# Optimization experiments

Measured on AMD Instinct MI355X. Metric: run time of the kernel, lower is better.

Reference implementation:

```python
import jax, jax.numpy as jnp
import numpy as np

GROUP = 64
DIM = 4096
N_HEADS = 32
N_KV = 8
HEAD_DIM = DIM // N_HEADS  # 128
N_REP = N_HEADS // N_KV    # 4
B = 1
S = 2048
THETA = 1e6


def _pack_q40(rng, out_f, in_f):
    """Random int4 weights packed Q4_0 style (two nibbles per int8) + per-group scales."""
    q = rng.integers(-7, 8, size=(out_f * in_f,)).reshape(-1, 2, GROUP)
    packed = ((q[:, 0] << 4) | (q[:, 1] & 15)).astype(np.int8)  # [out*in/group/2, group]
    scale = (np.abs(rng.standard_normal((out_f * in_f // GROUP, 1))) * 0.01 + 1e-3).astype(np.float32)
    return jnp.asarray(packed), jnp.asarray(scale)


def dequantize_q40(w, scale, shape):
    """Faithful port of torch dequantize_q40: arithmetic shifts sign-extend nibbles."""
    msb = jnp.right_shift(w, 4)                          # high nibble, sign-extended
    lsb = jnp.right_shift(jnp.left_shift(w, 4), 4)       # low nibble, sign-extended
    grp = jnp.concatenate([msb, lsb], axis=1).reshape(-1, GROUP)  # hstack then view(-1, group)
    return (grp.astype(scale.dtype) * scale).reshape(shape)


def setup_inputs() -> dict:
    rng = np.random.default_rng(0)
    wq, sq = _pack_q40(rng, N_HEADS * HEAD_DIM, DIM)
    wk, sk = _pack_q40(rng, N_KV * HEAD_DIM, DIM)
    wv, sv = _pack_q40(rng, N_KV * HEAD_DIM, DIM)
    wo, so = _pack_q40(rng, DIM, N_HEADS * HEAD_DIM)
    x = jnp.asarray(rng.standard_normal((B, S, DIM)), jnp.float32)
    inv_freq = 1.0 / (THETA ** (np.arange(0, HEAD_DIM, 2, dtype=np.float64) / HEAD_DIM))
    ang = np.outer(np.arange(S, dtype=np.float64), inv_freq)  # [S, HEAD_DIM/2]
    cos = jnp.asarray(np.cos(ang), jnp.float32)
    sin = jnp.asarray(np.sin(ang), jnp.float32)
    causal = np.triu(np.ones((S, S), dtype=bool), k=1)
    mask = jnp.asarray(np.where(causal, -1e9, 0.0), jnp.float32)
    return dict(x=x, wq=wq, sq=sq, wk=wk, sk=sk, wv=wv, sv=sv, wo=wo, so=so,
                cos=cos, sin=sin, mask=mask)


def _rotate_half(t):
    h = t.shape[-1] // 2
    return jnp.concatenate([-t[..., h:], t[..., :h]], axis=-1)


def reference(x, wq, sq, wk, sk, wv, sv, wo, so, cos, sin, mask):
    # Dequant-then-matmul QKV projections (weights stored as [out, in])
    Wq = dequantize_q40(wq, sq, (N_HEADS * HEAD_DIM, DIM))
    Wk = dequantize_q40(wk, sk, (N_KV * HEAD_DIM, DIM))
    Wv = dequantize_q40(wv, sv, (N_KV * HEAD_DIM, DIM))
    Wo = dequantize_q40(wo, so, (DIM, N_HEADS * HEAD_DIM))

    xq = (x @ Wq.T).reshape(B, S, N_HEADS, HEAD_DIM)
    xk = (x @ Wk.T).reshape(B, S, N_KV, HEAD_DIM)
    xv = (x @ Wv.T).reshape(B, S, N_KV, HEAD_DIM)

    # RoPE (rotate-half convention): cos/sin are [S, HEAD_DIM/2] -> cat to [S, HEAD_DIM]
    cosf = jnp.concatenate([cos, cos], axis=-1)[:, None, :]  # [S, 1, HEAD_DIM]
    sinf = jnp.concatenate([sin, sin], axis=-1)[:, None, :]
    xq = xq * cosf + _rotate_half(xq) * sinf
    xk = xk * cosf + _rotate_half(xk) * sinf

    # start_pos == 0 prefill: keys/values are the freshly projected xk/xv
    # GQA: repeat_interleave over the kv-head dim
    keys = jnp.repeat(xk, N_REP, axis=2)    # [B, S, N_HEADS, HEAD_DIM]
    values = jnp.repeat(xv, N_REP, axis=2)

    scores = jnp.einsum('bqhd,bkhd->bhqk', xq, keys) / np.float32(np.sqrt(HEAD_DIM))
    scores = scores + mask  # additive causal mask broadcast over [B, H]
    attn = jax.nn.softmax(scores, axis=-1)
    out = jnp.einsum('bhqk,bkhd->bqhd', attn, values).reshape(B, S, N_HEADS * HEAD_DIM)
    return out @ Wo.T
```

## Files before the change

### kernel.cpp

```cpp
#include <hip/hip_runtime.h>
#include <stdint.h>

#define DIMX 4096
#define NH   32
#define NKV  8
#define HD   128
#define SEQ  2048
#define QKVD 6144

typedef _Float16 h16;
typedef __attribute__((ext_vector_type(8))) _Float16 h16x8;
typedef __attribute__((ext_vector_type(4))) _Float16 h16x4;
typedef __attribute__((ext_vector_type(4))) float   f32x4;

__device__ __forceinline__ void gload_lds16(const void* g, void* l) {
  __builtin_amdgcn_global_load_lds(
      (const __attribute__((address_space(1))) void*)g,
      (__attribute__((address_space(3))) void*)l, 16, 0, 0);
}

template <int CTRL>
__device__ __forceinline__ float dpp_mv(float x) {
  int y = __builtin_amdgcn_mov_dpp(__builtin_bit_cast(int, x), CTRL, 0xF, 0xF, true);
  return __builtin_bit_cast(float, y);
}
__device__ __forceinline__ float red16_max(float x) {
  x = fmaxf(x, dpp_mv<0xB1>(x));
  x = fmaxf(x, dpp_mv<0x1B>(x));
  x = fmaxf(x, dpp_mv<0x141>(x));
  x = fmaxf(x, dpp_mv<0x140>(x));
  return x;
}
__device__ __forceinline__ float red16_sum(float x) {
  x += dpp_mv<0xB1>(x);
  x += dpp_mv<0x1B>(x);
  x += dpp_mv<0x141>(x);
  x += dpp_mv<0x140>(x);
  return x;
}

template <int PERM>
__device__ __forceinline__ void dq_unit(const void* __restrict__ w, const float* __restrict__ sc,
                                        h16* __restrict__ out, int u, int flag) {
  uint32_t b4;
  if (flag) {
    const int4 t = *(const int4*)((const int*)w + 4 * u);
    b4 = (uint32_t)(t.x & 0xFF) | ((uint32_t)(t.y & 0xFF) << 8) |
         ((uint32_t)(t.z & 0xFF) << 16) | ((uint32_t)(t.w & 0xFF) << 24);
  } else {
    b4 = ((const uint32_t*)w)[u];
  }
  int r = u >> 4;
  int p = (u & 15) * 4;
  float shi = sc[2 * r], slo = sc[2 * r + 1];
  h16x4 hi, lo;
#pragma unroll
  for (int j = 0; j < 4; ++j) {
    int by = (int)((b4 >> (8 * j)) & 0xFF);
    int hn = (by << 24) >> 28;
    int ln = (by << 28) >> 28;
    hi[j] = (h16)((float)hn * shi);
    lo[j] = (h16)((float)ln * slo);
  }
  size_t base;
  if (PERM) {
    int row  = r >> 5;
    int rowp = (row & ~127) | (((row & 63) << 1) | ((row >> 6) & 1));
    base = ((size_t)rowp << 12) + (size_t)((r & 31) << 7);
  } else {
    base = (size_t)r << 7;
  }
  *(h16x4*)(out + base + p)      = hi;
  *(h16x4*)(out + base + 64 + p) = lo;
}

#define U_WQ 2097152
#define U_WK 524288
#define U_WV 524288
#define U_WO 2097152

__global__ __launch_bounds__(256) void prep_all(
    const void* __restrict__ wq, const float* __restrict__ sq,
    const void* __restrict__ wk, const float* __restrict__ sk,
    const void* __restrict__ wv, const float* __restrict__ sv,
    const void* __restrict__ wo, const float* __restrict__ so,
    const float4* __restrict__ x,
    h16* __restrict__ Wqkv, h16* __restrict__ Wo, h16x4* __restrict__ xb) {
  __shared__ int sfl;
  if (threadIdx.x == 0) {
    int ok = 1;
    const int* wi = (const int*)wq;
    for (int i = 0; i < 64; ++i) {
      int v = wi[i];
      if (v < -128 || v > 127) ok = 0;
    }
    sfl = ok;
  }
  __syncthreads();
  const int fl = sfl;
  int u = blockIdx.x * 256 + threadIdx.x;
  if (u < U_WQ) { dq_unit<1>(wq, sq, Wqkv, u, fl); return; }
  u -= U_WQ;
  if (u < U_WK) { dq_unit<1>(wk, sk, Wqkv + 16777216, u, fl); return; }
  u -= U_WK;
  if (u < U_WV) { dq_unit<0>(wv, sv, Wqkv + 20971520, u, fl); return; }
  u -= U_WV;
  if (u < U_WO) { dq_unit<0>(wo, so, Wo, u, fl); return; }
  u -= U_WO;
  {
    float4 v = x[u];
    h16x4 o;
    o.x = (h16)v.x; o.y = (h16)v.y; o.z = (h16)v.z; o.w = (h16)v.w;
    xb[u] = o;
  }
}

template <typename OutT, int NT, int MODE>
__global__ __launch_bounds__(256) void gemm_bt(
    const h16* __restrict__ A, const h16* __restrict__ B,
    OutT* __restrict__ C, int M, int N, int K,
    const float* __restrict__ cosb, const float* __restrict__ sinb,
    h16* __restrict__ vt) {
  constexpr int BN = NT * 32;
  constexpr int SSZ = 128 * 64 + BN * 64;
  __shared__ __attribute__((aligned(16))) h16 SMEM[SSZ];
  h16* As = SMEM;
  h16* Bs = SMEM + 128 * 64;

  const int tid  = threadIdx.x;
  const int wv   = tid >> 6, lane = tid & 63;
  const int wr   = wv >> 1,  wc   = wv & 1;
  const int quad = lane >> 4, l15 = lane & 15;
  const int m0 = blockIdx.y * 128, n0 = blockIdx.x * BN;

  f32x4 acc[4][NT];
#pragma unroll
  for (int i = 0; i < 4; ++i)
#pragma unroll
    for (int j = 0; j < NT; ++j) acc[i][j] = (f32x4){0.f, 0.f, 0.f, 0.f};

  const h16* Ab = A + (size_t)m0 * K;
  const h16* Bb = B + (size_t)n0 * K;

  for (int k0 = 0; k0 < K; k0 += 64) {
    __syncthreads();
#pragma unroll
    for (int i = 0; i < 4; ++i) {
      int c = i * 256 + tid;
      int row = c >> 3, cs = c & 7, g = cs ^ (row & 7);
      gload_lds16(Ab + (size_t)row * K + k0 + g * 8, (char*)As + c * 16);
    }
#pragma unroll
    for (int i = 0; i < NT; ++i) {
      int c = i * 256 + tid;
      int row = c >> 3, cs = c & 7, g = cs ^ (row & 7);
      gload_lds16(Bb + (size_t)row * K + k0 + g * 8, (char*)Bs + c * 16);
    }
    __syncthreads();

#pragma unroll
    for (int ks = 0; ks < 2; ++ks) {
      h16x8 af[4], bfr[NT];
#pragma unroll
      for (int mt = 0; mt < 4; ++mt) {
        int row = wr * 64 + mt * 16 + l15;
        af[mt] = *(const h16x8*)&As[row * 64 + (((ks * 4 + quad) ^ (row & 7)) * 8)];
      }
#pragma unroll
      for (int nt = 0; nt < NT; ++nt) {
        int row = wc * (NT * 16) + nt * 16 + l15;
        bfr[nt] = *(const h16x8*)&Bs[row * 64 + (((ks * 4 + quad) ^ (row & 7)) * 8)];
      }
#pragma unroll
      for (int mt = 0; mt < 4; ++mt)
#pragma unroll
        for (int nt = 0; nt < NT; ++nt)
          acc[mt][nt] = __builtin_amdgcn_mfma_f32_16x16x32_f16(af[mt], bfr[nt], acc[mt][nt], 0, 0, 0);
    }
  }

#pragma unroll
  for (int mt = 0; mt < 4; ++mt)
#pragma unroll
    for (int nt = 0; nt < NT; ++nt)
#pragma unroll
      for (int r = 0; r < 4; ++r) {
        int row = m0 + wr * 64 + mt * 16 + quad * 4 + r;
        int col = n0 + wc * (NT * 16) + nt * 16 + l15;
        C[(size_t)row * N + col] = (OutT)acc[mt][nt][r];
      }
}

__global__ __launch_bounds__(512, 2) void gemm192_qkv(
    const h16* __restrict__ A, const h16* __restrict__ B, h16* __restrict__ C,
    const float* __restrict__ cosb, const float* __restrict__ sinb,
    h16* __restrict__ vt) {
  constexpr int K = DIMX;
  __shared__ __attribute__((aligned(16))) h16 SM[57344];

  const int tid  = threadIdx.x;
  const int w    = tid >> 6, lane = tid & 63;
  const int wr   = w >> 1, wc = w & 1;
  const int quad = lane >> 4, l15 = lane & 15;
  const int m0 = blockIdx.y * 256, n0 = blockIdx.x * 192;

  const h16* Ab = A + (size_t)m0 * K;
  const h16* Bb = B + (size_t)n0 * K;
  const int srow = tid >> 3;
  const int sg8  = ((tid & 7) ^ (srow & 7)) * 8;

  f32x4 acc[2][2][2][3];
#pragma unroll
  for (int a = 0; a < 2; ++a)
#pragma unroll
    for (int b = 0; b < 2; ++b)
#pragma unroll
      for (int mt = 0; mt < 2; ++mt)
#pragma unroll
        for (int nt = 0; nt < 3; ++nt) acc[a][b][mt][nt] = (f32x4){0.f, 0.f, 0.f, 0.f};

  h16x8 af[2][2];
  h16x8 bf[2][3][2];

#define STG(sl_, tile_) do {                                                        \
    const h16* g_ = ((sl_) < 4) ? (Ab + (size_t)((sl_) * 64) * K)                   \
                                : (Bb + (size_t)(((sl_) - 4) * 64) * K);            \
    char* d_ = (char*)(SM + ((tile_) & 1) * 28672 + (sl_) * 4096);                  \
    gload_lds16(g_ + (size_t)srow * K + (tile_) * 64 + sg8, d_ + tid * 16);         \
  } while (0)

#define LDA_(tile_, a_) do {                                                        \
    const h16* s_ = SM + ((tile_) & 1) * 28672 + wr * 4096;                         \
    _Pragma("unroll") for (int mt = 0; mt < 2; ++mt)                                \
    _Pragma("unroll") for (int ks = 0; ks < 2; ++ks) {                              \
      int row_ = (a_) * 32 + mt * 16 + l15;                                         \
      af[mt][ks] = *(const h16x8*)&s_[row_ * 64 + (((ks * 4 + quad) ^ (row_ & 7)) * 8)]; \
    }                                                                               \
  } while (0)

#define LDB_(tile_, b_) do {                                                        \
    const h16* s_ = SM + ((tile_) & 1) * 28672 + 16384;                             \
    _Pragma("unroll") for (int nt = 0; nt < 3; ++nt)                                \
    _Pragma("unroll") for (int ks = 0; ks < 2; ++ks) {                              \
      int row_ = (b_) * 96 + wc * 48 + nt * 16 + l15;                               \
      bf[b_][nt][ks] = *(const h16x8*)&s_[row_ * 64 + (((ks * 4 + quad) ^ (row_ & 7)) * 8)]; \
    }                                                                               \
  } while (0)

#define MMA_(a_, b_) do {                                                           \
    __builtin_amdgcn_s_setprio(1);                                                  \
    _Pragma("unroll") for (int mt = 0; mt < 2; ++mt)                                \
    _Pragma("unroll") for (int nt = 0; nt < 3; ++nt)                                \
    _Pragma("unroll") for (int ks = 0; ks < 2; ++ks)                                \
      acc[a_][b_][mt][nt] = __builtin_amdgcn_mfma_f32_16x16x32_f16(                 \
          af[mt][ks], bf[b_][nt][ks], acc[a_][b_][mt][nt], 0, 0, 0);                \
    __builtin_amdgcn_s_setprio(0);                                                  \
  } while (0)

#define CFENCE asm volatile("" ::: "memory")
#define BARX do { CFENCE; __builtin_amdgcn_s_barrier(); CFENCE; } while (0)
#define LG0  asm volatile("s_waitcnt lgkmcnt(0)" ::: "memory")
#define LKH8 asm volatile("s_waitcnt lgkmcnt(8)" ::: "memory")
#define VM5  asm volatile("s_waitcnt vmcnt(5)" ::: "memory")
#define VM0  asm volatile("s_waitcnt vmcnt(0)" ::: "memory")

  const int NT2 = K >> 6;

  STG(4, 0); STG(5, 0); STG(6, 0); STG(0, 0); STG(1, 0);
  STG(2, 0); STG(3, 0);
  STG(4, 1); STG(5, 1); STG(6, 1); STG(0, 1); STG(1, 1);
  VM5;
  BARX;

  for (int t = 0; t < NT2; ++t) {
    const int tp1 = (t + 1 < NT2) ? t + 1 : NT2 - 1;
    const int tp2 = (t + 2 < NT2) ? t + 2 : NT2 - 1;
    LDA_(t, 0); LDB_(t, 0);
    STG(2, tp1); STG(3, tp1);
    LKH8;
    BARX; LG0; MMA_(0, 0); BARX;
    LDB_(t, 1);
    STG(4, tp2);
    BARX; LG0; MMA_(0, 1); BARX;
    LDA_(t, 1);
    STG(5, tp2);
    BARX; LG0; MMA_(1, 1); BARX;
    STG(6, tp2); STG(0, tp2); STG(1, tp2);
    BARX; MMA_(1, 0); VM5; BARX;
  }
  VM0;

#pragma unroll
  for (int a = 0; a < 2; ++a)
#pragma unroll
    for (int b = 0; b < 2; ++b)
#pragma unroll
      for (int mt = 0; mt < 2; ++mt)
#pragma unroll
        for (int nt = 0; nt < 3; ++nt) {
          const int cb   = n0 + b * 96 + wc * 48 + nt * 16;
          const int row0 = m0 + wr * 64 + a * 32 + mt * 16 + quad * 4;
          if (cb >= 5120) {
            const int dcol = cb + l15 - 5120;
            h16x4 vvv;
#pragma unroll
            for (int r = 0; r < 4; ++r) vvv[r] = (h16)acc[a][b][mt][nt][r];
            *(h16x4*)(vt + (size_t)dcol * SEQ + row0) = vvv;
          } else {
            const int col = cb + l15;
            const int j   = (col & 127) >> 1;
            const float sgn = (col & 1) ? 1.f : -1.f;
#pragma unroll
            for (int r = 0; r < 4; ++r) {
              float own = acc[a][b][mt][nt][r];
              float par = dpp_mv<0xB1>(own);
              float cc  = cosb[(size_t)(row0 + r) * 64 + j];
              float ss  = sinb[(size_t)(row0 + r) * 64 + j];
              C[(size_t)(row0 + r) * QKVD + col] = (h16)(own * cc + sgn * par * ss);
            }
          }
        }
#undef STG
#undef LDA_
#undef LDB_
#undef MMA_
#undef CFENCE
#undef BARX
#undef LG0
#undef LKH8
#undef VM5
#undef VM0
}

__global__ __launch_bounds__(256, 2) void flash_attn(
    const h16* __restrict__ qkv, const h16* __restrict__ vt, h16* __restrict__ o_out) {
  __shared__ __attribute__((aligned(16))) h16 Ks[64 * 128];
  __shared__ __attribute__((aligned(16))) h16 Vts[128 * 64];
  __shared__ __attribute__((aligned(16))) h16 Ps[4][32 * 72];

  const int tid  = threadIdx.x;
  const int w    = tid >> 6, lane = tid & 63;
  const int quad = lane >> 4, l15 = lane & 15;
  const int h    = blockIdx.x;
  const int y    = blockIdx.y;
  const int qt   = (y < 8) ? (15 - y) : (y - 8);
  const int kv   = h >> 2;
  const int rowq = qt * 128 + w * 32;
  const h16* vtg = vt + (size_t)kv * HD * SEQ;

  h16x8 qf[2][4];
#pragma unroll
  for (int mt = 0; mt < 2; ++mt) {
    const h16* qrow = qkv + (size_t)(rowq + mt * 16 + l15) * QKVD + h * 128;
#pragma unroll
    for (int ks = 0; ks < 4; ++ks)
      qf[mt][ks] = *(const h16x8*)(qrow + ks * 32 + quad * 8);
  }

  f32x4 o[2][8];
#pragma unroll
  for (int mt = 0; mt < 2; ++mt)
#pragma unroll
    for (int i = 0; i < 8; ++i) o[mt][i] = (f32x4){0.f, 0.f, 0.f, 0.f};
  float mrow[2][4], lrow[2][4];
#pragma unroll
  for (int mt = 0; mt < 2; ++mt)
#pragma unroll
    for (int r = 0; r < 4; ++r) { mrow[mt][r] = -3e30f; lrow[mt][r] = 0.f; }
  h16* Psw = Ps[w];

  const int nkt = 2 * qt + 2;
  for (int kt = 0; kt < nkt; ++kt) {
    const int k0 = kt * 64;
    __syncthreads();
#pragma unroll
    for (int i = 0; i < 4; ++i) {
      int c = i * 256 + tid;
      int key = c >> 4, d8s = c & 15;
      gload_lds16(qkv + (size_t)(k0 + key) * QKVD + 4096 + kv * 128 + (d8s ^ (key & 15)) * 8,
                  (char*)Ks + c * 16);
    }
#pragma unroll
    for (int i = 0; i < 4; ++i) {
      int c = i * 256 + tid;
      int d = c >> 3, p = c & 7;
      gload_lds16(vtg + (size_t)d * SEQ + k0 + (p ^ (d & 7)) * 8,
                  (char*)Vts + c * 16);
    }
    __syncthreads();

    if (k0 <= rowq + 31) {
      const float sscale = 0.08838834764831845f;
      float alpha[2][4];
      f32x4 s2[2][4];
#pragma unroll
      for (int nt = 0; nt < 4; ++nt) {
        int key = nt * 16 + l15;
        f32x4 a0 = (f32x4){0.f, 0.f, 0.f, 0.f};
        f32x4 a1 = (f32x4){0.f, 0.f, 0.f, 0.f};
#pragma unroll
        for (int ks = 0; ks < 4; ++ks) {
          int d8 = ks * 4 + quad;
          h16x8 kf = *(const h16x8*)&Ks[key * 128 + ((d8 ^ (key & 15)) * 8)];
          a0 = __builtin_amdgcn_mfma_f32_16x16x32_f16(qf[0][ks], kf, a0, 0, 0, 0);
          a1 = __builtin_amdgcn_mfma_f32_16x16x32_f16(qf[1][ks], kf, a1, 0, 0, 0);
        }
        s2[0][nt] = a0;
        s2[1][nt] = a1;
      }
#pragma unroll
      for (int mt = 0; mt < 2; ++mt) {
#pragma unroll
        for (int r = 0; r < 4; ++r) {
          int rowg = rowq + mt * 16 + quad * 4 + r;
          float pv[4];
          float tm = -3e30f;
#pragma unroll
          for (int nt = 0; nt < 4; ++nt) {
            float v = s2[mt][nt][r] * sscale;
            if (k0 + nt * 16 + l15 > rowg) v = -3e30f;
            pv[nt] = v;
            tm = fmaxf(tm, v);
          }
          tm = red16_max(tm);
          float mnew = fmaxf(mrow[mt][r], tm);
          float a = __expf(mrow[mt][r] - mnew);
          mrow[mt][r] = mnew;
          alpha[mt][r] = a;
          float ps = 0.f;
#pragma unroll
          for (int nt = 0; nt < 4; ++nt) {
            float e = __expf(pv[nt] - mnew);
            ps += e;
            Psw[(mt * 16 + quad * 4 + r) * 72 + nt * 16 + l15] = (h16)e;
          }
          ps = red16_sum(ps);
          lrow[mt][r] = lrow[mt][r] * a + ps;
        }
      }
#pragma unroll
      for (int mt = 0; mt < 2; ++mt)
#pragma unroll
        for (int on = 0; on < 8; ++on) {
          o[mt][on][0] *= alpha[mt][0]; o[mt][on][1] *= alpha[mt][1];
          o[mt][on][2] *= alpha[mt][2]; o[mt][on][3] *= alpha[mt][3];
        }
      asm volatile("s_waitcnt lgkmcnt(0)" ::: "memory");
#pragma unroll
      for (int ks = 0; ks < 2; ++ks) {
        h16x8 pf0 = *(const h16x8*)&Psw[(0  + l15) * 72 + ks * 32 + quad * 8];
        h16x8 pf1 = *(const h16x8*)&Psw[(16 + l15) * 72 + ks * 32 + quad * 8];
        int k8 = ks * 4 + quad;
#pragma unroll
        for (int on = 0; on < 8; ++on) {
          int d = on * 16 + l15;
          h16x8 vf = *(const h16x8*)&Vts[d * 64 + ((k8 ^ (d & 7)) * 8)];
          o[0][on] = __builtin_amdgcn_mfma_f32_16x16x32_f16(pf0, vf, o[0][on], 0, 0, 0);
          o[1][on] = __builtin_amdgcn_mfma_f32_16x16x32_f16(pf1, vf, o[1][on], 0, 0, 0);
        }
      }
    }
  }
#pragma unroll
  for (int mt = 0; mt < 2; ++mt) {
    float linv[4];
#pragma unroll
    for (int r = 0; r < 4; ++r) linv[r] = 1.0f / lrow[mt][r];
#pragma unroll
    for (int on = 0; on < 8; ++on)
#pragma unroll
      for (int r = 0; r < 4; ++r) {
        int row = rowq + mt * 16 + quad * 4 + r;
        int col = h * 128 + on * 16 + l15;
        o_out[(size_t)row * DIMX + col] = (h16)(o[mt][on][r] * linv[r]);
      }
  }
}

extern "C" void kernel_launch(void* const* d_in, const int* in_sizes, int n_in,
                              void* d_out, int out_size, void* d_ws, size_t ws_size,
                              hipStream_t stream) {
  const float* x    = (const float*)d_in[0];
  const void*  wq   = d_in[1];
  const float* sq   = (const float*)d_in[2];
  const void*  wk   = d_in[3];
  const float* sk   = (const float*)d_in[4];
  const void*  wv   = d_in[5];
  const float* sv   = (const float*)d_in[6];
  const void*  wo   = d_in[7];
  const float* so   = (const float*)d_in[8];
  const float* cosb = (const float*)d_in[9];
  const float* sinb = (const float*)d_in[10];
  float* out = (float*)d_out;

  char* ws = (char*)d_ws;
  h16* Wqkv = (h16*)ws;
  h16* Wo   = (h16*)(ws + 50331648);
  h16* xb   = (h16*)(ws + 83886080);
  h16* qkv  = (h16*)(ws + 100663296);
  h16* vt   = (h16*)d_out;

  prep_all<<<28672, 256, 0, stream>>>(wq, sq, wk, sk, wv, sv, wo, so,
                                      (const float4*)x, Wqkv, Wo, (h16x4*)xb);

  gemm192_qkv<<<dim3(32, 8), 512, 0, stream>>>(xb, Wqkv, qkv, cosb, sinb, vt);

  flash_attn<<<dim3(32, 16), 256, 0, stream>>>(qkv, vt, xb);

  gemm_bt<float, 4, 0><<<dim3(32, 16), 256, 0, stream>>>(
      xb, Wo, out, SEQ, DIMX, DIMX, cosb, sinb, vt);
}
```

Before: 457.8 us.

## Unify GEMMs into templated software-pipelined kernel and use it for output projection

Replaces the simple single-buffered output-projection GEMM with a templated version of the double-buffered, barrier-interleaved QKV GEMM, now using 256x128 tiles and 512 threads. The main loop is restructured to process two K-tiles per iteration, with ping-pong B-fragment registers and finer vmcnt waits, so LDS reads, global-to-LDS loads and MFMAs overlap more closely. The goal is to hide memory latency in both projections, especially the Wo GEMM that previously synchronized twice per tile without prefetch. In exchange the new schedule is more complex, relies on hand-tuned waitcnt values and higher register pressure, and a miscounted wait could cause stalls or wrong results.

```diff
diff --git a/kernel.cpp b/kernel.cpp
--- a/kernel.cpp
+++ b/kernel.cpp
@@ -116,100 +116,28 @@
 }
 
 template <typename OutT, int NT, int MODE>
-__global__ __launch_bounds__(256) void gemm_bt(
-    const h16* __restrict__ A, const h16* __restrict__ B,
-    OutT* __restrict__ C, int M, int N, int K,
+__global__ __launch_bounds__(512, 2) void gemm_pipe(
+    const h16* __restrict__ A, const h16* __restrict__ B, OutT* __restrict__ C,
+    int N, int K,
     const float* __restrict__ cosb, const float* __restrict__ sinb,
     h16* __restrict__ vt) {
-  constexpr int BN = NT * 32;
-  constexpr int SSZ = 128 * 64 + BN * 64;
-  __shared__ __attribute__((aligned(16))) h16 SMEM[SSZ];
-  h16* As = SMEM;
-  h16* Bs = SMEM + 128 * 64;
-
-  const int tid  = threadIdx.x;
-  const int wv   = tid >> 6, lane = tid & 63;
-  const int wr   = wv >> 1,  wc   = wv & 1;
-  const int quad = lane >> 4, l15 = lane & 15;
-  const int m0 = blockIdx.y * 128, n0 = blockIdx.x * BN;
-
-  f32x4 acc[4][NT];
-#pragma unroll
-  for (int i = 0; i < 4; ++i)
-#pragma unroll
-    for (int j = 0; j < NT; ++j) acc[i][j] = (f32x4){0.f, 0.f, 0.f, 0.f};
-
-  const h16* Ab = A + (size_t)m0 * K;
-  const h16* Bb = B + (size_t)n0 * K;
-
-  for (int k0 = 0; k0 < K; k0 += 64) {
-    __syncthreads();
-#pragma unroll
-    for (int i = 0; i < 4; ++i) {
-      int c = i * 256 + tid;
-      int row = c >> 3, cs = c & 7, g = cs ^ (row & 7);
-      gload_lds16(Ab + (size_t)row * K + k0 + g * 8, (char*)As + c * 16);
-    }
-#pragma unroll
-    for (int i = 0; i < NT; ++i) {
-      int c = i * 256 + tid;
-      int row = c >> 3, cs = c & 7, g = cs ^ (row & 7);
-      gload_lds16(Bb + (size_t)row * K + k0 + g * 8, (char*)Bs + c * 16);
-    }
-    __syncthreads();
-
-#pragma unroll
-    for (int ks = 0; ks < 2; ++ks) {
-      h16x8 af[4], bfr[NT];
-#pragma unroll
-      for (int mt = 0; mt < 4; ++mt) {
-        int row = wr * 64 + mt * 16 + l15;
-        af[mt] = *(const h16x8*)&As[row * 64 + (((ks * 4 + quad) ^ (row & 7)) * 8)];
-      }
-#pragma unroll
-      for (int nt = 0; nt < NT; ++nt) {
-        int row = wc * (NT * 16) + nt * 16 + l15;
-        bfr[nt] = *(const h16x8*)&Bs[row * 64 + (((ks * 4 + quad) ^ (row & 7)) * 8)];
-      }
-#pragma unroll
-      for (int mt = 0; mt < 4; ++mt)
-#pragma unroll
-        for (int nt = 0; nt < NT; ++nt)
-          acc[mt][nt] = __builtin_amdgcn_mfma_f32_16x16x32_f16(af[mt], bfr[nt], acc[mt][nt], 0, 0, 0);
-    }
-  }
-
-#pragma unroll
-  for (int mt = 0; mt < 4; ++mt)
-#pragma unroll
-    for (int nt = 0; nt < NT; ++nt)
-#pragma unroll
-      for (int r = 0; r < 4; ++r) {
-        int row = m0 + wr * 64 + mt * 16 + quad * 4 + r;
-        int col = n0 + wc * (NT * 16) + nt * 16 + l15;
-        C[(size_t)row * N + col] = (OutT)acc[mt][nt][r];
-      }
-}
-
-__global__ __launch_bounds__(512, 2) void gemm192_qkv(
-    const h16* __restrict__ A, const h16* __restrict__ B, h16* __restrict__ C,
-    const float* __restrict__ cosb, const float* __restrict__ sinb,
-    h16* __restrict__ vt) {
-  constexpr int K = DIMX;
-  __shared__ __attribute__((aligned(16))) h16 SM[57344];
+  constexpr int NSLOT = 4 + NT;
+  constexpr int BUFH  = NSLOT * 4096;
+  __shared__ __attribute__((aligned(16))) h16 SM[2 * BUFH];
 
   const int tid  = threadIdx.x;
   const int w    = tid >> 6, lane = tid & 63;
   const int wr   = w >> 1, wc = w & 1;
   const int quad = lane >> 4, l15 = lane & 15;
-  const int m0 = blockIdx.y * 256, n0 = blockIdx.x * 192;
+  const int axr  = l15 & 7;
+  const int m0 = blockIdx.y * 256, n0 = blockIdx.x * (NT * 64);
 
   const h16* Ab = A + (size_t)m0 * K;
   const h16* Bb = B + (size_t)n0 * K;
   const int srow = tid >> 3;
   const int sg8  = ((tid & 7) ^ (srow & 7)) * 8;
 
-  f32x4 acc[2][2][2][3];
+  f32x4 acc[2][2][2][NT];
 #pragma unroll
   for (int a = 0; a < 2; ++a)
 #pragma unroll
@@ -217,118 +145,181 @@
 #pragma unroll
       for (int mt = 0; mt < 2; ++mt)
 #pragma unroll
-        for (int nt = 0; nt < 3; ++nt) acc[a][b][mt][nt] = (f32x4){0.f, 0.f, 0.f, 0.f};
-
-  h16x8 af[2][2];
-  h16x8 bf[2][3][2];
+        for (int nt = 0; nt < NT; ++nt) acc[a][b][mt][nt] = (f32x4){0.f, 0.f, 0.f, 0.f};
+
+  h16x8 af[2][2][2];
+  h16x8 bf1[NT][2];
+  h16x8 bf0E[NT][2], bf0O[NT][2];
 
 #define STG(sl_, tile_) do {                                                        \
     const h16* g_ = ((sl_) < 4) ? (Ab + (size_t)((sl_) * 64) * K)                   \
                                 : (Bb + (size_t)(((sl_) - 4) * 64) * K);            \
-    char* d_ = (char*)(SM + ((tile_) & 1) * 28672 + (sl_) * 4096);                  \
+    char* d_ = (char*)(SM + ((tile_) & 1) * BUFH + (sl_) * 4096);                   \
     gload_lds16(g_ + (size_t)srow * K + (tile_) * 64 + sg8, d_ + tid * 16);         \
   } while (0)
 
 #define LDA_(tile_, a_) do {                                                        \
-    const h16* s_ = SM + ((tile_) & 1) * 28672 + wr * 4096;                         \
+    const h16* s_ = SM + ((tile_) & 1) * BUFH + wr * 4096;                          \
     _Pragma("unroll") for (int mt = 0; mt < 2; ++mt)                                \
-    _Pragma("unroll") for (int ks = 0; ks < 2; ++ks) {                              \
-      int row_ = (a_) * 32 + mt * 16 + l15;                                         \
-      af[mt][ks] = *(const h16x8*)&s_[row_ * 64 + (((ks * 4 + quad) ^ (row_ & 7)) * 8)]; \
-    }                                                                               \
+    _Pragma("unroll") for (int ks = 0; ks < 2; ++ks)                                \
+      af[a_][mt][ks] = *(const h16x8*)&s_[((a_) * 32 + mt * 16 + l15) * 64 +        \
+                                          (((ks * 4 + quad) ^ axr) * 8)];           \
   } while (0)
 
-#define LDB_(tile_, b_) do {                                                        \
-    const h16* s_ = SM + ((tile_) & 1) * 28672 + 16384;                             \
-    _Pragma("unroll") for (int nt = 0; nt < 3; ++nt)                                \
-    _Pragma("unroll") for (int ks = 0; ks < 2; ++ks) {                              \
-      int row_ = (b_) * 96 + wc * 48 + nt * 16 + l15;                               \
-      bf[b_][nt][ks] = *(const h16x8*)&s_[row_ * 64 + (((ks * 4 + quad) ^ (row_ & 7)) * 8)]; \
-    }                                                                               \
+#define LDB1_(tile_) do {                                                           \
+    const h16* s_ = SM + ((tile_) & 1) * BUFH + 16384;                              \
+    _Pragma("unroll") for (int nt = 0; nt < NT; ++nt)                               \
+    _Pragma("unroll") for (int ks = 0; ks < 2; ++ks)                                \
+      bf1[nt][ks] = *(const h16x8*)&s_[(NT * 32 + wc * (NT * 16) + nt * 16 + l15) * 64 + \
+                                       (((ks * 4 + quad) ^ axr) * 8)];              \
   } while (0)
 
-#define MMA_(a_, b_) do {                                                           \
+#define LDB0_(tile_, D_) do {                                                       \
+    const h16* s_ = SM + ((tile_) & 1) * BUFH + 16384;                              \
+    _Pragma("unroll") for (int nt = 0; nt < NT; ++nt)                               \
+    _Pragma("unroll") for (int ks = 0; ks < 2; ++ks)                                \
+      D_[nt][ks] = *(const h16x8*)&s_[(wc * (NT * 16) + nt * 16 + l15) * 64 +       \
+                                      (((ks * 4 + quad) ^ axr) * 8)];               \
+  } while (0)
+
+#define MMAB1(a_) do {                                                              \
     __builtin_amdgcn_s_setprio(1);                                                  \
     _Pragma("unroll") for (int mt = 0; mt < 2; ++mt)                                \
-    _Pragma("unroll") for (int nt = 0; nt < 3; ++nt)                                \
+    _Pragma("unroll") for (int nt = 0; nt < NT; ++nt)                               \
     _Pragma("unroll") for (int ks = 0; ks < 2; ++ks)                                \
-      acc[a_][b_][mt][nt] = __builtin_amdgcn_mfma_f32_16x16x32_f16(                 \
-          af[mt][ks], bf[b_][nt][ks], acc[a_][b_][mt][nt], 0, 0, 0);                \
+      acc[a_][1][mt][nt] = __builtin_amdgcn_mfma_f32_16x16x32_f16(                  \
+          af[a_][mt][ks], bf1[nt][ks], acc[a_][1][mt][nt], 0, 0, 0);                \
     __builtin_amdgcn_s_setprio(0);                                                  \
   } while (0)
 
+#define MMAB0(a_, D_) do {                                                          \
+    __builtin_amdgcn_s_setprio(1);                                                  \
+    _Pragma("unroll") for (int mt = 0; mt < 2; ++mt)                                \
+    _Pragma("unroll") for (int nt = 0; nt < NT; ++nt)                               \
+    _Pragma("unroll") for (int ks = 0; ks < 2; ++ks)                                \
+      acc[a_][0][mt][nt] = __builtin_amdgcn_mfma_f32_16x16x32_f16(                  \
+          af[a_][mt][ks], D_[nt][ks], acc[a_][0][mt][nt], 0, 0, 0);                 \
+    __builtin_amdgcn_s_setprio(0);                                                  \
+  } while (0)
+
 #define CFENCE asm volatile("" ::: "memory")
 #define BARX do { CFENCE; __builtin_amdgcn_s_barrier(); CFENCE; } while (0)
-#define LG0  asm volatile("s_waitcnt lgkmcnt(0)" ::: "memory")
-#define LKH8 asm volatile("s_waitcnt lgkmcnt(8)" ::: "memory")
 #define VM5  asm volatile("s_waitcnt vmcnt(5)" ::: "memory")
+#define VM2  asm volatile("s_waitcnt vmcnt(2)" ::: "memory")
+#define VMP4 do { if constexpr (NT == 3) asm volatile("s_waitcnt vmcnt(2)" ::: "memory"); \
+                  else                   asm volatile("s_waitcnt vmcnt(1)" ::: "memory"); } while (0)
 #define VM0  asm volatile("s_waitcnt vmcnt(0)" ::: "memory")
 
-  const int NT2 = K >> 6;
-
-  STG(4, 0); STG(5, 0); STG(6, 0); STG(0, 0); STG(1, 0);
-  STG(2, 0); STG(3, 0);
-  STG(4, 1); STG(5, 1); STG(6, 1); STG(0, 1); STG(1, 1);
-  VM5;
+  const int NTILE = K >> 6;
+  const int NIT   = K >> 7;
+
+  if constexpr (NT == 3) {
+    STG(4, 0); STG(5, 0); STG(0, 0); STG(1, 0); STG(2, 0); STG(3, 0); STG(6, 0);
+    STG(4, 1); STG(5, 1);
+    VMP4;
+  } else {
+    STG(4, 0); STG(0, 0); STG(1, 0); STG(2, 0); STG(3, 0); STG(5, 0);
+    STG(4, 1);
+    VMP4;
+  }
   BARX;
-
-  for (int t = 0; t < NT2; ++t) {
-    const int tp1 = (t + 1 < NT2) ? t + 1 : NT2 - 1;
-    const int tp2 = (t + 2 < NT2) ? t + 2 : NT2 - 1;
-    LDA_(t, 0); LDB_(t, 0);
-    STG(2, tp1); STG(3, tp1);
-    LKH8;
-    BARX; LG0; MMA_(0, 0); BARX;
-    LDB_(t, 1);
-    STG(4, tp2);
-    BARX; LG0; MMA_(0, 1); BARX;
-    LDA_(t, 1);
-    STG(5, tp2);
-    BARX; LG0; MMA_(1, 1); BARX;
-    STG(6, tp2); STG(0, tp2); STG(1, tp2);
-    BARX; MMA_(1, 0); VM5; BARX;
+  LDA_(0, 0); LDB0_(0, bf0E);
+
+  for (int i = 0; i < NIT; ++i) {
+    const int t0 = 2 * i, t1 = 2 * i + 1;
+    const int T2 = (t0 + 2 < NTILE) ? t0 + 2 : NTILE - 1;
+    const int T3 = (t1 + 2 < NTILE) ? t1 + 2 : NTILE - 1;
+    LDB1_(t0);
+    STG(0, t1); STG(1, t1); STG(2, t1); STG(3, t1);
+    MMAB0(0, bf0E); BARX;
+    LDA_(t0, 1);
+    if constexpr (NT == 3) STG(6, t1); else STG(5, t1);
+    VM5;
+    MMAB1(0); BARX;
+    LDB0_(t1, bf0O);
+    STG(4, T2);
+    VM2;
+    MMAB1(1); BARX;
+    LDA_(t1, 0);
+    if constexpr (NT == 3) STG(5, T2);
+    VMP4;
+    MMAB0(1, bf0E); BARX;
+    LDB1_(t1);
+    STG(0, T2); STG(1, T2); STG(2, T2); STG(3, T2);
+    MMAB0(0, bf0O); BARX;
+    LDA_(t1, 1);
+    if constexpr (NT == 3) STG(6, T2); else STG(5, T2);
+    VM5;
+    MMAB1(0); BARX;
+    LDB0_(T2, bf0E);
+    STG(4, T3);
+    VM2;
+    MMAB1(1); BARX;
+    LDA_(T2, 0);
+    if constexpr (NT == 3) STG(5, T3);
+    VMP4;
+    MMAB0(1, bf0O); BARX;
   }
   VM0;
 
-#pragma unroll
-  for (int a = 0; a < 2; ++a)
-#pragma unroll
-    for (int b = 0; b < 2; ++b)
-#pragma unroll
-      for (int mt = 0; mt < 2; ++mt)
-#pragma unroll
-        for (int nt = 0; nt < 3; ++nt) {
-          const int cb   = n0 + b * 96 + wc * 48 + nt * 16;
-          const int row0 = m0 + wr * 64 + a * 32 + mt * 16 + quad * 4;
-          if (cb >= 5120) {
-            const int dcol = cb + l15 - 5120;
-            h16x4 vvv;
-#pragma unroll
-            for (int r = 0; r < 4; ++r) vvv[r] = (h16)acc[a][b][mt][nt][r];
-            *(h16x4*)(vt + (size_t)dcol * SEQ + row0) = vvv;
-          } else {
-            const int col = cb + l15;
-            const int j   = (col & 127) >> 1;
-            const float sgn = (col & 1) ? 1.f : -1.f;
-#pragma unroll
-            for (int r = 0; r < 4; ++r) {
-              float own = acc[a][b][mt][nt][r];
-              float par = dpp_mv<0xB1>(own);
-              float cc  = cosb[(size_t)(row0 + r) * 64 + j];
-              float ss  = sinb[(size_t)(row0 + r) * 64 + j];
-              C[(size_t)(row0 + r) * QKVD + col] = (h16)(own * cc + sgn * par * ss);
+  if constexpr (MODE == 1) {
+#pragma unroll
+    for (int a = 0; a < 2; ++a)
+#pragma unroll
+      for (int b = 0; b < 2; ++b)
+#pragma unroll
+        for (int mt = 0; mt < 2; ++mt)
+#pragma unroll
+          for (int nt = 0; nt < NT; ++nt) {
+            const int cb   = n0 + b * (NT * 32) + wc * (NT * 16) + nt * 16;
+            const int row0 = m0 + wr * 64 + a * 32 + mt * 16 + quad * 4;
+            if (cb >= 5120) {
+              const int dcol = cb + l15 - 5120;
+              h16x4 vvv;
+#pragma unroll
+              for (int r = 0; r < 4; ++r) vvv[r] = (h16)acc[a][b][mt][nt][r];
+              *(h16x4*)(vt + (size_t)dcol * SEQ + row0) = vvv;
+            } else {
+              const int col = cb + l15;
+              const int j   = (col & 127) >> 1;
+              const float sgn = (col & 1) ? 1.f : -1.f;
+#pragma unroll
+              for (int r = 0; r < 4; ++r) {
+                float own = acc[a][b][mt][nt][r];
+                float par = dpp_mv<0xB1>(own);
+                float cc  = cosb[(size_t)(row0 + r) * 64 + j];
+                float ss  = sinb[(size_t)(row0 + r) * 64 + j];
+                C[(size_t)(row0 + r) * N + col] = (OutT)(own * cc + sgn * par * ss);
+              }
             }
           }
-        }
+  } else {
+#pragma unroll
+    for (int a = 0; a < 2; ++a)
+#pragma unroll
+      for (int b = 0; b < 2; ++b)
+#pragma unroll
+        for (int mt = 0; mt < 2; ++mt)
+#pragma unroll
+          for (int nt = 0; nt < NT; ++nt)
+#pragma unroll
+            for (int r = 0; r < 4; ++r) {
+              int row = m0 + wr * 64 + a * 32 + mt * 16 + quad * 4 + r;
+              int col = n0 + b * (NT * 32) + wc * (NT * 16) + nt * 16 + l15;
+              C[(size_t)row * N + col] = (OutT)acc[a][b][mt][nt][r];
+            }
+  }
 #undef STG
 #undef LDA_
-#undef LDB_
-#undef MMA_
+#undef LDB1_
+#undef LDB0_
+#undef MMAB1
+#undef MMAB0
 #undef CFENCE
 #undef BARX
-#undef LG0
-#undef LKH8
 #undef VM5
+#undef VM2
+#undef VMP4
 #undef VM0
 }
 
@@ -503,10 +494,11 @@
   prep_all<<<28672, 256, 0, stream>>>(wq, sq, wk, sk, wv, sv, wo, so,
                                       (const float4*)x, Wqkv, Wo, (h16x4*)xb);
 
-  gemm192_qkv<<<dim3(32, 8), 512, 0, stream>>>(xb, Wqkv, qkv, cosb, sinb, vt);
+  gemm_pipe<h16, 3, 1><<<dim3(32, 8), 512, 0, stream>>>(
+      xb, Wqkv, qkv, QKVD, DIMX, cosb, sinb, vt);
 
   flash_attn<<<dim3(32, 16), 256, 0, stream>>>(qkv, vt, xb);
 
-  gemm_bt<float, 4, 0><<<dim3(32, 16), 256, 0, stream>>>(
-      xb, Wo, out, SEQ, DIMX, DIMX, cosb, sinb, vt);
-}
+  gemm_pipe<float, 2, 0><<<dim3(32, 8), 512, 0, stream>>>(
+      xb, Wo, out, DIMX, DIMX, cosb, sinb, vt);
+}
```

Result: faster. 433.4 us (-5.3%).
